# Kernel optimization log

Measured on AMD Instinct MI355X. Metric: run time of the kernel, lower is better.

## Reference

```python
import jax, jax.numpy as jnp
import numpy as np

B, S, I, E, D = 64, 512, 64, 256, 256  # batch, src_len, input_size, enc_hid, dec_hid


def _lstm_cell(h, c, x, Wih, Whh, b):
    # PyTorch LSTM gate order: i, f, g, o ; b = b_ih + b_hh combined
    z = x @ Wih.T + h @ Whh.T + b
    i, f, g, o = jnp.split(z, 4, axis=-1)
    c = jax.nn.sigmoid(f) * c + jax.nn.sigmoid(i) * jnp.tanh(g)
    h = jax.nn.sigmoid(o) * jnp.tanh(c)
    return h, c


def _run_lstm(x, h0, c0, Wih, Whh, b):
    # x: [B,S,I] -> outputs [B,S,H]
    def step(carry, xt):
        h, c = _lstm_cell(carry[0], carry[1], xt, Wih, Whh, b)
        return (h, c), h
    _, ys = jax.lax.scan(step, (h0, c0), jnp.swapaxes(x, 0, 1))
    return jnp.swapaxes(ys, 0, 1)


def _forward(x, enc_h0, enc_c0, dec_h0, dec_c0, Wih_f, Whh_f, b_f, Wih_b, Whh_b, b_b,
             W_attn, b_attn, v, Wih_d, Whh_d, b_d, W_lin, b_lin):
    b_, s_ = x.shape[0], x.shape[1]
    # bidirectional encoder
    out_f = _run_lstm(x, enc_h0[0], enc_c0[0], Wih_f, Whh_f, b_f)
    out_b = _run_lstm(x[:, ::-1, :], enc_h0[1], enc_c0[1], Wih_b, Whh_b, b_b)[:, ::-1, :]
    enc_out = jnp.concatenate([out_f, out_b], axis=-1)  # [B,S,2E]
    h0d, c0d = dec_h0[0], dec_c0[0]  # decoder re-starts from these EVERY step (faithful)

    @jax.checkpoint
    def dec_step(carry, _):
        y, h_attn = carry  # y: [B,1], h_attn: [B,D]
        dh = h_attn.shape[-1]
        cat = jnp.concatenate(
            [jnp.broadcast_to(h_attn[:, None, :], (b_, s_, dh)), enc_out], axis=-1)
        energy = jnp.tanh(cat @ W_attn.T + b_attn)              # [B,S,D]
        attn = jax.nn.softmax(jnp.einsum('d,bsd->bs', v, energy), axis=1)
        context = jnp.einsum('bs,bse->be', attn, enc_out)       # [B,2E]
        dec_in = jnp.concatenate([y, context], axis=-1)         # [B,1+2E]
        h_new, _c = _lstm_cell(h0d, c0d, dec_in, Wih_d, Whh_d, b_d)
        y_new = jnp.concatenate([h_new, context], axis=-1) @ W_lin.T + b_lin  # [B,1]
        return (y_new, h_new), y_new

    y0 = jnp.zeros((b_, 1), dtype=x.dtype)
    _, ys = jax.lax.scan(dec_step, (y0, h0d), None, length=s_)  # [S,B,1]
    # output_size == 1, so torch's cat-then-[:,1:] equals the stacked per-step ys
    return jnp.swapaxes(ys, 0, 1).reshape(b_, s_)


def setup_inputs() -> dict:
    key = jax.random.key(0)
    ks = jax.random.split(key, 20)
    W = 0.05  # weight scale ~ torch default init magnitude
    rn = lambda k, sh, s: jax.random.normal(k, sh, dtype=jnp.float32) * s
    return {
        'x': rn(ks[0], (B, S, I), 1.0),
        'enc_h0': rn(ks[1], (2, B, E), 1.0),
        'enc_c0': rn(ks[2], (2, B, E), 1.0),
        'dec_h0': rn(ks[3], (1, B, D), 1.0),
        'dec_c0': rn(ks[4], (1, B, D), 1.0),
        'Wih_f': rn(ks[5], (4 * E, I), W),
        'Whh_f': rn(ks[6], (4 * E, E), W),
        'b_f': rn(ks[7], (4 * E,), W),
        'Wih_b': rn(ks[8], (4 * E, I), W),
        'Whh_b': rn(ks[9], (4 * E, E), W),
        'b_b': rn(ks[10], (4 * E,), W),
        'W_attn': rn(ks[11], (D, D + 2 * E), W),
        'b_attn': rn(ks[12], (D,), W),
        'v': jax.random.uniform(ks[13], (D,), dtype=jnp.float32),
        'Wih_d': rn(ks[14], (4 * D, 2 * E + 1), W),
        'Whh_d': rn(ks[15], (4 * D, D), W),
        'b_d': rn(ks[16], (4 * D,), W),
        'W_lin': rn(ks[17], (1, 2 * E + D), W),
        'b_lin': rn(ks[18], (1,), W),
    }


def reference(x, enc_h0, enc_c0, dec_h0, dec_c0, Wih_f, Whh_f, b_f, Wih_b, Whh_b, b_b,
              W_attn, b_attn, v, Wih_d, Whh_d, b_d, W_lin, b_lin):
    return _forward(x, enc_h0, enc_c0, dec_h0, dec_c0, Wih_f, Whh_f, b_f,
                    Wih_b, Whh_b, b_b, W_attn, b_attn, v, Wih_d, Whh_d, b_d,
                    W_lin, b_lin)
```

## Files before the change

### kernel.cpp

```cpp
#include <hip/hip_runtime.h>
#include <hip/hip_bf16.h>

#define NB 64
#define NS 512
#define NI 64
#define NE 256
#define ND 256
#define N4E 1024
#define N4D 1024
#define NTE 512
#define G 4
#define SLICE 128
#define CELLS 64

__device__ __forceinline__ float fsig(float x){
    return __fdividef(1.f, 1.f + __expf(-x));
}
__device__ __forceinline__ float ftanh(float x){
    x = fminf(10.f, fmaxf(-10.f, x));
    float e = __expf(2.f*x);
    return 1.f - __fdividef(2.f, e + 1.f);
}
__device__ __forceinline__ float wave_sum(float v){
    #pragma unroll
    for (int o=32;o>0;o>>=1) v += __shfl_xor(v, o, 64);
    return v;
}
__device__ __forceinline__ float wave_max(float v){
    #pragma unroll
    for (int o=32;o>0;o>>=1) v = fmaxf(v, __shfl_xor(v, o, 64));
    return v;
}
__device__ __forceinline__ float blo(unsigned u){ return __uint_as_float(u<<16); }
__device__ __forceinline__ float bhi(unsigned u){ return __uint_as_float(u & 0xffff0000u); }
__device__ __forceinline__ unsigned short bfbits(float f){
    __hip_bfloat16 h = __float2bfloat16(f);
    return *(unsigned short*)&h;
}
__device__ __forceinline__ float ld_agf(const float* p){
    return __hip_atomic_load(p, __ATOMIC_RELAXED, __HIP_MEMORY_SCOPE_AGENT);
}
__device__ __forceinline__ void st_agf(float* p, float v){
    __hip_atomic_store(p, v, __ATOMIC_RELAXED, __HIP_MEMORY_SCOPE_AGENT);
}

__device__ __forceinline__ void groupbar(unsigned* flags, int b, int q,
                                         unsigned tgt, int tid){
    __syncthreads();
    if (tid == 0)
        __hip_atomic_store(&flags[b*4+q], tgt, __ATOMIC_RELAXED, __HIP_MEMORY_SCOPE_AGENT);
    if (tid < 4){
        while (__hip_atomic_load(&flags[b*4+tid], __ATOMIC_RELAXED,
                                 __HIP_MEMORY_SCOPE_AGENT) < tgt)
            __builtin_amdgcn_s_sleep(1);
    }
    __syncthreads();
}

__global__ void k_transpose(float* __restrict__ dst, const float* __restrict__ src,
                            int R, int C, int ld, int off){
    int idx = blockIdx.x*256 + threadIdx.x;
    if (idx >= R*C) return;
    int r = idx / C, c = idx - r*C;
    dst[(size_t)c*R + r] = src[(size_t)r*ld + off + c];
}
__global__ void k_transpose16(__hip_bfloat16* __restrict__ dst, const float* __restrict__ src,
                              int R, int C, int ld, int off){
    int idx = blockIdx.x*256 + threadIdx.x;
    if (idx >= R*C) return;
    int r = idx / C, c = idx - r*C;
    dst[(size_t)c*R + r] = __float2bfloat16(src[(size_t)r*ld + off + c]);
}

__global__ void k_pack_wy(float* __restrict__ wy, const float* __restrict__ Wih_d){
    int j = blockIdx.x*256 + threadIdx.x;
    if (j < N4D) wy[j] = Wih_d[(size_t)j*(NTE+1)];
}

__global__ void k_pack_wdtg(__hip_bfloat16* __restrict__ dst, const float* __restrict__ Wih_d){
    int idx = blockIdx.x*256 + threadIdx.x;
    int q = idx >> 17, rem = idx & 131071;
    int e = rem >> 8, jj = rem & 255;
    int j = ((jj>>6)<<8) + (q<<6) + (jj&63);
    dst[idx] = __float2bfloat16(Wih_d[(size_t)j*(NTE+1) + 1 + e]);
}

__global__ void k_zc(float* __restrict__ zc, const float* __restrict__ WhhTd,
                     const float* __restrict__ h0d, const float* __restrict__ b_d){
    int b = blockIdx.x, tid = threadIdx.x;
    __shared__ float h0[ND];
    if (tid < ND) h0[tid] = h0d[b*ND + tid];
    __syncthreads();
    for (int j = tid; j < N4D; j += 256){
        float acc = b_d[j];
        #pragma unroll 8
        for (int d=0; d<ND; ++d) acc = fmaf(h0[d], WhhTd[d*N4D + j], acc);
        zc[b*N4D + j] = acc;
    }
}

__global__ void k_dec_init(float* __restrict__ hG, float* __restrict__ yG,
                           unsigned* __restrict__ flags, const float* __restrict__ dec_h0){
    int b = blockIdx.x, tid = threadIdx.x;
    hG[b*ND + tid] = dec_h0[b*ND + tid];
    if (tid < G) yG[b*G + tid] = 0.f;
    if (tid < G) flags[b*G + tid] = 0u;
}

__global__ __launch_bounds__(1024) void k_enc(
    const float* __restrict__ x, const float* __restrict__ eh0, const float* __restrict__ ec0,
    const unsigned* __restrict__ whhTf, const unsigned* __restrict__ wihTf, const float* __restrict__ bf,
    const unsigned* __restrict__ whhTb, const unsigned* __restrict__ wihTb, const float* __restrict__ bb,
    unsigned* __restrict__ eo32)
{
    int bid = blockIdx.x;
    int b = bid & 63, dir = bid >> 6;
    int tid = threadIdx.x;
    int j2 = tid & 511, kh = tid >> 9;
    const unsigned* whh = dir ? whhTb : whhTf;
    const unsigned* wih = dir ? wihTb : wihTf;
    const float* bias = dir ? bb : bf;

    __shared__ __align__(16) float h_l[NE];
    __shared__ __align__(16) float xt[2][NI];
    __shared__ float zp0[N4E], zp1[N4E];

    float2 bias2 = make_float2(0.f, 0.f);
    if (kh == 0) bias2 = ((const float2*)bias)[j2];

    float cst = 0.f;
    if (tid < NE){
        h_l[tid] = eh0[(dir*NB+b)*NE + tid];
        cst      = ec0[(dir*NB+b)*NE + tid];
    }
    {
        int st0 = dir ? (NS-1) : 0;
        if (tid < 16) ((float4*)xt[0])[tid] = ((const float4*)(x + ((size_t)b*NS+st0)*NI))[tid];
    }
    __syncthreads();

    const unsigned* wihK = wih + (size_t)(kh*32)*512 + j2;
    const unsigned* whhK = whh + (size_t)(kh*128)*512 + j2;
    float* zpme = kh ? zp1 : zp0;

    for (int t=0;t<NS;++t){
        int st = dir ? (NS-1-t) : t;
        float4 xpre = make_float4(0.f,0.f,0.f,0.f);
        if (t+1 < NS && tid < 16){
            int stn = dir ? (NS-2-t) : (t+1);
            xpre = ((const float4*)(x + ((size_t)b*NS+stn)*NI))[tid];
        }
        const float* xc = xt[t&1];
        float x0=bias2.x, y0=bias2.y, x1=0.f, y1=0.f;
        #pragma unroll 8
        for (int ii=0; ii<32; ii+=2){
            int i = kh*32 + ii;
            unsigned wa = wihK[(size_t)ii*512];
            unsigned wb = wihK[(size_t)(ii+1)*512];
            float xa = xc[i], xb = xc[i+1];
            x0 = fmaf(xa, blo(wa), x0); y0 = fmaf(xa, bhi(wa), y0);
            x1 = fmaf(xb, blo(wb), x1); y1 = fmaf(xb, bhi(wb), y1);
        }
        #pragma unroll 8
        for (int dd=0; dd<128; dd+=2){
            int d = kh*128 + dd;
            unsigned wa = whhK[(size_t)dd*512];
            unsigned wb = whhK[(size_t)(dd+1)*512];
            float ha = h_l[d], hb = h_l[d+1];
            x0 = fmaf(ha, blo(wa), x0); y0 = fmaf(ha, bhi(wa), y0);
            x1 = fmaf(hb, blo(wb), x1); y1 = fmaf(hb, bhi(wb), y1);
        }
        ((float2*)zpme)[j2] = make_float2(x0+x1, y0+y1);
        if (t+1 < NS && tid < 16) ((float4*)xt[(t+1)&1])[tid] = xpre;
        __syncthreads();
        if (tid < NE){
            int c = tid;
            float zi = zp0[c]        + zp1[c];
            float zf = zp0[NE+c]     + zp1[NE+c];
            float zg = zp0[2*NE+c]   + zp1[2*NE+c];
            float zo = zp0[3*NE+c]   + zp1[3*NE+c];
            cst = fsig(zf)*cst + fsig(zi)*ftanh(zg);
            float hn = fsig(zo)*ftanh(cst);
            h_l[c] = hn;
            ((unsigned short*)eo32)[((size_t)b*NS+st)*NTE + dir*NE + c] = bfbits(hn);
        }
        __syncthreads();
    }
}

__global__ __launch_bounds__(256) void k_encproj(const unsigned* __restrict__ eo32,
        const float* __restrict__ WeT, const float* __restrict__ b_attn,
        unsigned short* __restrict__ ep_pk16){
    int b = blockIdx.y, s0 = blockIdx.x*16, tid = threadIdx.x;
    __shared__ float tile[16*NTE];
    {
        const unsigned* eop = eo32 + (size_t)(b*NS + s0)*256;
        for (int k=0;k<32;++k){
            int wi = k*256 + tid;
            unsigned w = eop[wi];
            int sl = wi>>8, ew = wi&255;
            tile[sl*NTE + 2*ew]   = blo(w);
            tile[sl*NTE + 2*ew+1] = bhi(w);
        }
    }
    __syncthreads();
    float acc[16];
    float ba = b_attn[tid];
    #pragma unroll
    for (int sl=0;sl<16;++sl) acc[sl]=ba;
    #pragma unroll 4
    for (int e4=0;e4<128;++e4){
        float w0 = WeT[(4*e4+0)*ND+tid];
        float w1 = WeT[(4*e4+1)*ND+tid];
        float w2 = WeT[(4*e4+2)*ND+tid];
        float w3 = WeT[(4*e4+3)*ND+tid];
        #pragma unroll
        for (int sl=0;sl<16;++sl){
            const float4 tv = *(const float4*)&tile[sl*NTE + 4*e4];
            acc[sl] = fmaf(tv.x,w0,fmaf(tv.y,w1,fmaf(tv.z,w2,fmaf(tv.w,w3,acc[sl]))));
        }
    }
    #pragma unroll
    for (int sl=0;sl<16;++sl){
        int s = s0+sl;
        size_t wdi = ((size_t)(b*4 + (s>>7))*128 + (tid>>1))*128 + (s&127);
        ep_pk16[wdi*2 + (tid&1)] = bfbits(acc[sl]);
    }
}

__global__ __launch_bounds__(1024, 4) void k_dec(
    const unsigned* __restrict__ eo32,
    const unsigned* __restrict__ ep_pk,
    const unsigned* __restrict__ WhTp,
    const float* __restrict__ v,
    const float* __restrict__ zc, const float* __restrict__ wy,
    const unsigned* __restrict__ WdTp_all,
    const float* __restrict__ dec_c0,
    const float* __restrict__ W_lin, const float* __restrict__ b_lin,
    float* __restrict__ hG, float* __restrict__ yG,
    float* __restrict__ ctxG, float* __restrict__ msG,
    unsigned* __restrict__ flags,
    float* __restrict__ out)
{
    int bid = blockIdx.x;
    int b = bid & 63, q = bid >> 6;
    int tid = threadIdx.x;

    __shared__ unsigned ep_lds[16384];
    __shared__ float part[2048];
    __shared__ float h_l[ND];
    __shared__ float2 hv[ND];
    __shared__ float v_l[ND];
    __shared__ float scores_l[SLICE];
    __shared__ float ctx_l[NTE];
    __shared__ float z_l[256], zc_l[256], wy_l[256];
    __shared__ float c0_l[CELLS], wlh_l[CELLS], wlc_l[SLICE];
    __shared__ float msbuf[8];
    __shared__ float wred[16];
    __shared__ float smax, yprev;

    const unsigned* WdTp = WdTp_all + (size_t)q*NTE*128;

    for (int i=tid; i<16384; i+=1024)
        ep_lds[i] = ep_pk[(size_t)(b*4+q)*16384 + i];
    unsigned eo_reg[32];
    {
        int ep2 = tid & 255, sq = tid >> 8;
        const unsigned* eop = eo32 + (size_t)(b*NS + q*SLICE + sq*32)*256 + ep2;
        #pragma unroll
        for (int ss=0; ss<32; ++ss) eo_reg[ss] = eop[(size_t)ss*256];
    }
    if (tid < 256){
        int jj = tid;
        int j = ((jj>>6)<<8) + (q<<6) + (jj&63);
        zc_l[jj] = zc[b*N4D + j];
        wy_l[jj] = wy[j];
        v_l[tid] = v[tid];
    }
    if (tid < CELLS){
        c0_l[tid]  = dec_c0[b*ND + q*CELLS + tid];
        wlh_l[tid] = W_lin[q*CELLS + tid];
    }
    if (tid < SLICE) wlc_l[tid] = W_lin[ND + q*SLICE + tid];
    float blin = b_lin[0];
    __syncthreads();

    for (int t=0; t<NS; ++t){
        if (tid < ND) h_l[tid] = ld_agf(&hG[b*ND + tid]);
        if (tid == 0){
            float y = 0.f;
            if (t > 0){
                y = blin + ld_agf(&yG[b*G+0]) + ld_agf(&yG[b*G+1])
                         + ld_agf(&yG[b*G+2]) + ld_agf(&yG[b*G+3]);
                if (q == 0) out[(size_t)b*NS + (t-1)] = y;
            }
            yprev = y;
        }
        __syncthreads();
        {
            int d2 = tid & 127, kq = tid >> 7;
            float ax = 0.f, ay = 0.f;
            #pragma unroll 8
            for (int kk=0; kk<32; ++kk){
                int k = kq*32 + kk;
                unsigned w = WhTp[k*128 + d2];
                float hvv = h_l[k];
                ax = fmaf(hvv, blo(w), ax); ay = fmaf(hvv, bhi(w), ay);
            }
            ((float2*)part)[kq*128 + d2] = make_float2(ax, ay);
        }
        __syncthreads();
        if (tid < ND){
            float s = 0.f;
            #pragma unroll
            for (int r=0;r<8;++r) s += part[r*256 + tid];
            hv[tid] = make_float2(v_l[tid], s);
        }
        __syncthreads();
        {
            int sl = tid & 127, dg = tid >> 7;
            float sc = 0.f;
            const unsigned* epl = ep_lds + dg*16*128 + sl;
            #pragma unroll
            for (int k16=0; k16<16; ++k16){
                unsigned w = epl[k16*128];
                int d = dg*32 + 2*k16;
                float2 a0 = hv[d], a1 = hv[d+1];
                sc += a0.x*ftanh(blo(w) + a0.y) + a1.x*ftanh(bhi(w) + a1.y);
            }
            part[dg*128 + sl] = sc;
        }
        __syncthreads();
        if (tid < SLICE){
            float s = 0.f;
            #pragma unroll
            for (int r=0;r<8;++r) s += part[r*128 + tid];
            part[1024 + tid] = s;
            float wm = wave_max(s);
            if ((tid&63)==0) wred[tid>>6] = wm;
        }
        __syncthreads();
        if (tid == 0) smax = fmaxf(wred[0], wred[1]);
        __syncthreads();
        if (tid < SLICE){
            float ev = __expf(part[1024 + tid] - smax);
            scores_l[tid] = ev;
            float s = wave_sum(ev);
            if ((tid&63)==0) wred[2+(tid>>6)] = s;
        }
        __syncthreads();
        if (tid == 0){
            st_agf(&msG[(b*G+q)*2+0], smax);
            st_agf(&msG[(b*G+q)*2+1], wred[2]+wred[3]);
        }
        {
            int ep2 = tid & 255, sq = tid >> 8;
            float ax = 0.f, ay = 0.f;
            #pragma unroll
            for (int ss=0; ss<32; ++ss){
                unsigned w = eo_reg[ss];
                float sc = scores_l[sq*32 + ss];
                ax = fmaf(sc, blo(w), ax); ay = fmaf(sc, bhi(w), ay);
            }
            ((float2*)part)[sq*256 + ep2] = make_float2(ax, ay);
        }
        __syncthreads();
        if (tid < NTE){
            float s = part[tid] + part[512+tid] + part[1024+tid] + part[1536+tid];
            st_agf(&ctxG[(size_t)(b*G+q)*NTE + tid], s);
        }
        groupbar(flags, b, q, (unsigned)(2*t+1), tid);
        float cg0=0.f, cg1=0.f, cg2=0.f, cg3=0.f;
        if (tid < 2*G) msbuf[tid] = ld_agf(&msG[b*G*2 + tid]);
        if (tid < NTE){
            const float* cg = ctxG + (size_t)b*G*NTE + tid;
            cg0 = ld_agf(cg);        cg1 = ld_agf(cg+NTE);
            cg2 = ld_agf(cg+2*NTE);  cg3 = ld_agf(cg+3*NTE);
        }
        __syncthreads();
        float mm = fmaxf(fmaxf(msbuf[0], msbuf[2]), fmaxf(msbuf[4], msbuf[6]));
        float w0 = __expf(msbuf[0]-mm), w1 = __expf(msbuf[2]-mm),
              w2 = __expf(msbuf[4]-mm), w3 = __expf(msbuf[6]-mm);
        float inv = __fdividef(1.f, msbuf[1]*w0 + msbuf[3]*w1 + msbuf[5]*w2 + msbuf[7]*w3);
        if (tid < NTE)
            ctx_l[tid] = (cg0*w0 + cg1*w1 + cg2*w2 + cg3*w3) * inv;
        __syncthreads();
        {
            int jj2 = tid & 127, eq = tid >> 7;
            float ax = 0.f, ay = 0.f;
            #pragma unroll 8
            for (int ee=0; ee<64; ++ee){
                int e = eq*64 + ee;
                unsigned w = WdTp[e*128 + jj2];
                float cv = ctx_l[e];
                ax = fmaf(cv, blo(w), ax); ay = fmaf(cv, bhi(w), ay);
            }
            ((float2*)part)[eq*128 + jj2] = make_float2(ax, ay);
        }
        __syncthreads();
        if (tid < 256){
            float s = zc_l[tid] + yprev*wy_l[tid];
            #pragma unroll
            for (int r=0;r<8;++r) s += part[r*256 + tid];
            z_l[tid] = s;
        }
        __syncthreads();
        float yp = 0.f;
        if (tid < CELLS){
            float zi=z_l[tid], zf=z_l[64+tid], zg=z_l[128+tid], zo=z_l[192+tid];
            float cn = fsig(zf)*c0_l[tid] + fsig(zi)*ftanh(zg);
            float hn = fsig(zo)*ftanh(cn);
            st_agf(&hG[b*ND + q*CELLS + tid], hn);
            yp = hn * wlh_l[tid];
        } else if (tid < CELLS + SLICE){
            yp = ctx_l[q*SLICE + (tid - CELLS)] * wlc_l[tid - CELLS];
        }
        {
            float s = wave_sum(yp);
            if ((tid&63)==0 && tid < 192) wred[8+(tid>>6)] = s;
        }
        __syncthreads();
        if (tid == 0) st_agf(&yG[b*G + q], wred[8]+wred[9]+wred[10]);
        groupbar(flags, b, q, (unsigned)(2*t+2), tid);
    }
    if (q == 0 && tid == 0){
        out[(size_t)b*NS + (NS-1)] = blin + ld_agf(&yG[b*G+0]) + ld_agf(&yG[b*G+1])
                                          + ld_agf(&yG[b*G+2]) + ld_agf(&yG[b*G+3]);
    }
}

extern "C" void kernel_launch(void* const* d_in, const int* in_sizes, int n_in,
                              void* d_out, int out_size, void* d_ws, size_t ws_size,
                              hipStream_t stream){
    const float* x      = (const float*)d_in[0];
    const float* enc_h0 = (const float*)d_in[1];
    const float* enc_c0 = (const float*)d_in[2];
    const float* dec_h0 = (const float*)d_in[3];
    const float* dec_c0 = (const float*)d_in[4];
    const float* Wih_f  = (const float*)d_in[5];
    const float* Whh_f  = (const float*)d_in[6];
    const float* b_f    = (const float*)d_in[7];
    const float* Wih_b  = (const float*)d_in[8];
    const float* Whh_b  = (const float*)d_in[9];
    const float* b_b    = (const float*)d_in[10];
    const float* W_attn = (const float*)d_in[11];
    const float* b_attn = (const float*)d_in[12];
    const float* v      = (const float*)d_in[13];
    const float* Wih_d  = (const float*)d_in[14];
    const float* Whh_d  = (const float*)d_in[15];
    const float* b_d    = (const float*)d_in[16];
    const float* W_lin  = (const float*)d_in[17];
    const float* b_lin  = (const float*)d_in[18];
    float* out = (float*)d_out;
    char* ws   = (char*)d_ws;

    size_t off = 0;
    auto alloc = [&](size_t bytes)->size_t{ size_t o = off; off += (bytes + 255) & ~(size_t)255; return o; };
    size_t o_eo16   = alloc((size_t)NB*NS*NTE*2);
    size_t o_eppk   = alloc((size_t)NB*G*128*128*4);
    size_t o_WihTf  = alloc((size_t)NI*N4E*2);
    size_t o_WhhTf  = alloc((size_t)NE*N4E*2);
    size_t o_WihTb  = alloc((size_t)NI*N4E*2);
    size_t o_WhhTb  = alloc((size_t)NE*N4E*2);
    size_t o_WhT16  = alloc((size_t)ND*ND*2);
    size_t o_WeT    = alloc((size_t)NTE*ND*4);
    size_t o_WdTg   = alloc((size_t)G*NTE*256*2);
    size_t o_WhhTd  = alloc((size_t)ND*N4D*4);
    size_t o_zc     = alloc((size_t)NB*N4D*4);
    size_t o_wy     = alloc((size_t)N4D*4);
    size_t o_hG     = alloc((size_t)NB*ND*4);
    size_t o_yG     = alloc((size_t)NB*G*4);
    size_t o_ctxG   = alloc((size_t)NB*G*NTE*4);
    size_t o_msG    = alloc((size_t)NB*G*2*4);
    size_t o_flags  = alloc((size_t)NB*G*4);
    if (ws_size < off) return;

    auto F   = [&](size_t o)->float*{ return (float*)(ws + o); };
    auto U32 = [&](size_t o)->unsigned*{ return (unsigned*)(ws + o); };
    auto H16 = [&](size_t o)->__hip_bfloat16*{ return (__hip_bfloat16*)(ws + o); };

    auto T32 = [&](size_t dsto, const float* src, int R, int C, int ld, int offc){
        int n = R*C;
        k_transpose<<<dim3((n+255)/256), dim3(256), 0, stream>>>(F(dsto), src, R, C, ld, offc);
    };
    auto T16 = [&](size_t dsto, const float* src, int R, int C, int ld, int offc){
        int n = R*C;
        k_transpose16<<<dim3((n+255)/256), dim3(256), 0, stream>>>(H16(dsto), src, R, C, ld, offc);
    };
    T16(o_WihTf, Wih_f, N4E, NI, NI, 0);
    T16(o_WhhTf, Whh_f, N4E, NE, NE, 0);
    T16(o_WihTb, Wih_b, N4E, NI, NI, 0);
    T16(o_WhhTb, Whh_b, N4E, NE, NE, 0);
    T16(o_WhT16, W_attn, ND, ND, ND+NTE, 0);
    T32(o_WeT,   W_attn, ND, NTE, ND+NTE, ND);
    T32(o_WhhTd, Whh_d, N4D, ND, ND, 0);
    k_pack_wdtg<<<dim3((G*NTE*256)/256), dim3(256), 0, stream>>>(H16(o_WdTg), Wih_d);
    k_pack_wy<<<dim3(4), dim3(256), 0, stream>>>(F(o_wy), Wih_d);
    k_zc<<<dim3(NB), dim3(256), 0, stream>>>(F(o_zc), F(o_WhhTd), dec_h0, b_d);
    k_dec_init<<<dim3(NB), dim3(256), 0, stream>>>(F(o_hG), F(o_yG), (unsigned*)(ws+o_flags), dec_h0);

    k_enc<<<dim3(2*NB), dim3(1024), 0, stream>>>(x, enc_h0, enc_c0,
        U32(o_WhhTf), U32(o_WihTf), b_f, U32(o_WhhTb), U32(o_WihTb), b_b, U32(o_eo16));

    k_encproj<<<dim3(NS/16, NB), dim3(256), 0, stream>>>(U32(o_eo16), F(o_WeT), b_attn,
        (unsigned short*)(ws+o_eppk));

    k_dec<<<dim3(NB*G), dim3(1024), 0, stream>>>(U32(o_eo16), U32(o_eppk),
        U32(o_WhT16), v, F(o_zc), F(o_wy), U32(o_WdTg), dec_c0, W_lin, b_lin,
        F(o_hG), F(o_yG), F(o_ctxG), F(o_msG), (unsigned*)(ws+o_flags), out);
}
```

Baseline: 18.35 ms.

## Run decoder with one block per batch, dropping cross-block barriers

The decoder's per-batch work is no longer split across four cooperating blocks that synchronise through global flags and atomics twice per step. One 1024-thread block now handles a whole batch row with uint4-vectorised bf16 weight loads, and softmax and context are reduced locally. This removes the inter-block barrier latency and global traffic on every step. In exchange only 64 blocks run, encoder outputs stream from global or L2 instead of living in registers or LDS, and per-block work grows fourfold. The tanh clamp is also dropped.

```diff
diff --git a/kernel.cpp b/kernel.cpp
--- a/kernel.cpp
+++ b/kernel.cpp
@@ -9,17 +9,12 @@
 #define N4E 1024
 #define N4D 1024
 #define NTE 512
-#define G 4
-#define SLICE 128
-#define CELLS 64
 
 __device__ __forceinline__ float fsig(float x){
     return __fdividef(1.f, 1.f + __expf(-x));
 }
 __device__ __forceinline__ float ftanh(float x){
-    x = fminf(10.f, fmaxf(-10.f, x));
-    float e = __expf(2.f*x);
-    return 1.f - __fdividef(2.f, e + 1.f);
+    return 1.f - __fdividef(2.f, 1.f + __expf(2.f*x));
 }
 __device__ __forceinline__ float wave_sum(float v){
     #pragma unroll
@@ -36,25 +31,6 @@
 __device__ __forceinline__ unsigned short bfbits(float f){
     __hip_bfloat16 h = __float2bfloat16(f);
     return *(unsigned short*)&h;
-}
-__device__ __forceinline__ float ld_agf(const float* p){
-    return __hip_atomic_load(p, __ATOMIC_RELAXED, __HIP_MEMORY_SCOPE_AGENT);
-}
-__device__ __forceinline__ void st_agf(float* p, float v){
-    __hip_atomic_store(p, v, __ATOMIC_RELAXED, __HIP_MEMORY_SCOPE_AGENT);
-}
-
-__device__ __forceinline__ void groupbar(unsigned* flags, int b, int q,
-                                         unsigned tgt, int tid){
-    __syncthreads();
-    if (tid == 0)
-        __hip_atomic_store(&flags[b*4+q], tgt, __ATOMIC_RELAXED, __HIP_MEMORY_SCOPE_AGENT);
-    if (tid < 4){
-        while (__hip_atomic_load(&flags[b*4+tid], __ATOMIC_RELAXED,
-                                 __HIP_MEMORY_SCOPE_AGENT) < tgt)
-            __builtin_amdgcn_s_sleep(1);
-    }
-    __syncthreads();
 }
 
 __global__ void k_transpose(float* __restrict__ dst, const float* __restrict__ src,
@@ -75,14 +51,6 @@
 __global__ void k_pack_wy(float* __restrict__ wy, const float* __restrict__ Wih_d){
     int j = blockIdx.x*256 + threadIdx.x;
     if (j < N4D) wy[j] = Wih_d[(size_t)j*(NTE+1)];
-}
-
-__global__ void k_pack_wdtg(__hip_bfloat16* __restrict__ dst, const float* __restrict__ Wih_d){
-    int idx = blockIdx.x*256 + threadIdx.x;
-    int q = idx >> 17, rem = idx & 131071;
-    int e = rem >> 8, jj = rem & 255;
-    int j = ((jj>>6)<<8) + (q<<6) + (jj&63);
-    dst[idx] = __float2bfloat16(Wih_d[(size_t)j*(NTE+1) + 1 + e]);
 }
 
 __global__ void k_zc(float* __restrict__ zc, const float* __restrict__ WhhTd,
@@ -97,14 +65,6 @@
         for (int d=0; d<ND; ++d) acc = fmaf(h0[d], WhhTd[d*N4D + j], acc);
         zc[b*N4D + j] = acc;
     }
-}
-
-__global__ void k_dec_init(float* __restrict__ hG, float* __restrict__ yG,
-                           unsigned* __restrict__ flags, const float* __restrict__ dec_h0){
-    int b = blockIdx.x, tid = threadIdx.x;
-    hG[b*ND + tid] = dec_h0[b*ND + tid];
-    if (tid < G) yG[b*G + tid] = 0.f;
-    if (tid < G) flags[b*G + tid] = 0u;
 }
 
 __global__ __launch_bounds__(1024) void k_enc(
@@ -223,209 +183,198 @@
     #pragma unroll
     for (int sl=0;sl<16;++sl){
         int s = s0+sl;
-        size_t wdi = ((size_t)(b*4 + (s>>7))*128 + (tid>>1))*128 + (s&127);
+        size_t wdi = ((size_t)(b*128) + (tid>>1))*NS + s;
         ep_pk16[wdi*2 + (tid&1)] = bfbits(acc[sl]);
     }
 }
 
-__global__ __launch_bounds__(1024, 4) void k_dec(
-    const unsigned* __restrict__ eo32,
-    const unsigned* __restrict__ ep_pk,
-    const unsigned* __restrict__ WhTp,
+__global__ __launch_bounds__(1024, 1) void k_dec(
+    const uint4* __restrict__ eo4,
+    const uint4* __restrict__ ep4,
+    const uint4* __restrict__ whT4,
+    const uint4* __restrict__ wdT4,
     const float* __restrict__ v,
     const float* __restrict__ zc, const float* __restrict__ wy,
-    const unsigned* __restrict__ WdTp_all,
-    const float* __restrict__ dec_c0,
+    const float* __restrict__ dec_h0, const float* __restrict__ dec_c0,
     const float* __restrict__ W_lin, const float* __restrict__ b_lin,
-    float* __restrict__ hG, float* __restrict__ yG,
-    float* __restrict__ ctxG, float* __restrict__ msG,
-    unsigned* __restrict__ flags,
     float* __restrict__ out)
 {
-    int bid = blockIdx.x;
-    int b = bid & 63, q = bid >> 6;
-    int tid = threadIdx.x;
-
-    __shared__ unsigned ep_lds[16384];
-    __shared__ float part[2048];
+    int b = blockIdx.x, tid = threadIdx.x;
+
+    __shared__ float part[8192];
+    __shared__ float2 hv[ND];
     __shared__ float h_l[ND];
-    __shared__ float2 hv[ND];
-    __shared__ float v_l[ND];
-    __shared__ float scores_l[SLICE];
+    __shared__ float scores_l[NS];
     __shared__ float ctx_l[NTE];
-    __shared__ float z_l[256], zc_l[256], wy_l[256];
-    __shared__ float c0_l[CELLS], wlh_l[CELLS], wlc_l[SLICE];
-    __shared__ float msbuf[8];
+    __shared__ float z_l[N4D], zc_l[N4D], wy_l[N4D];
+    __shared__ float c0_l[ND], wlh_l[ND], wlc_l[NTE];
     __shared__ float wred[16];
-    __shared__ float smax, yprev;
-
-    const unsigned* WdTp = WdTp_all + (size_t)q*NTE*128;
-
-    for (int i=tid; i<16384; i+=1024)
-        ep_lds[i] = ep_pk[(size_t)(b*4+q)*16384 + i];
-    unsigned eo_reg[32];
-    {
-        int ep2 = tid & 255, sq = tid >> 8;
-        const unsigned* eop = eo32 + (size_t)(b*NS + q*SLICE + sq*32)*256 + ep2;
-        #pragma unroll
-        for (int ss=0; ss<32; ++ss) eo_reg[ss] = eop[(size_t)ss*256];
-    }
-    if (tid < 256){
-        int jj = tid;
-        int j = ((jj>>6)<<8) + (q<<6) + (jj&63);
-        zc_l[jj] = zc[b*N4D + j];
-        wy_l[jj] = wy[j];
-        v_l[tid] = v[tid];
-    }
-    if (tid < CELLS){
-        c0_l[tid]  = dec_c0[b*ND + q*CELLS + tid];
-        wlh_l[tid] = W_lin[q*CELLS + tid];
-    }
-    if (tid < SLICE) wlc_l[tid] = W_lin[ND + q*SLICE + tid];
+    __shared__ float yprevS;
+
+    zc_l[tid] = zc[b*N4D + tid];
+    wy_l[tid] = wy[tid];
+    if (tid < ND){
+        hv[tid]    = make_float2(v[tid], 0.f);
+        h_l[tid]   = dec_h0[b*ND + tid];
+        c0_l[tid]  = dec_c0[b*ND + tid];
+        wlh_l[tid] = W_lin[tid];
+    }
+    if (tid < NTE) wlc_l[tid] = W_lin[ND + tid];
+    if (tid == 0) yprevS = 0.f;
     float blin = b_lin[0];
     __syncthreads();
 
+    const uint4* epb = ep4 + (size_t)b*128*128;
+    const uint4* eob = eo4 + (size_t)b*NS*64;
+
     for (int t=0; t<NS; ++t){
-        if (tid < ND) h_l[tid] = ld_agf(&hG[b*ND + tid]);
-        if (tid == 0){
-            float y = 0.f;
-            if (t > 0){
-                y = blin + ld_agf(&yG[b*G+0]) + ld_agf(&yG[b*G+1])
-                         + ld_agf(&yG[b*G+2]) + ld_agf(&yG[b*G+3]);
-                if (q == 0) out[(size_t)b*NS + (t-1)] = y;
-            }
-            yprev = y;
-        }
-        __syncthreads();
-        {
-            int d2 = tid & 127, kq = tid >> 7;
-            float ax = 0.f, ay = 0.f;
-            #pragma unroll 8
-            for (int kk=0; kk<32; ++kk){
-                int k = kq*32 + kk;
-                unsigned w = WhTp[k*128 + d2];
+        {
+            int d4 = tid & 31, kq = tid >> 5;
+            float ax[8];
+            #pragma unroll
+            for (int j=0;j<8;++j) ax[j]=0.f;
+            #pragma unroll
+            for (int kk=0; kk<8; ++kk){
+                int k = kq*8 + kk;
+                uint4 w = whT4[k*32 + d4];
                 float hvv = h_l[k];
-                ax = fmaf(hvv, blo(w), ax); ay = fmaf(hvv, bhi(w), ay);
-            }
-            ((float2*)part)[kq*128 + d2] = make_float2(ax, ay);
+                ax[0]=fmaf(hvv,blo(w.x),ax[0]); ax[1]=fmaf(hvv,bhi(w.x),ax[1]);
+                ax[2]=fmaf(hvv,blo(w.y),ax[2]); ax[3]=fmaf(hvv,bhi(w.y),ax[3]);
+                ax[4]=fmaf(hvv,blo(w.z),ax[4]); ax[5]=fmaf(hvv,bhi(w.z),ax[5]);
+                ax[6]=fmaf(hvv,blo(w.w),ax[6]); ax[7]=fmaf(hvv,bhi(w.w),ax[7]);
+            }
+            #pragma unroll
+            for (int j=0;j<8;++j) part[kq*256 + d4*8 + j] = ax[j];
         }
         __syncthreads();
         if (tid < ND){
             float s = 0.f;
             #pragma unroll
-            for (int r=0;r<8;++r) s += part[r*256 + tid];
-            hv[tid] = make_float2(v_l[tid], s);
-        }
-        __syncthreads();
-        {
-            int sl = tid & 127, dg = tid >> 7;
-            float sc = 0.f;
-            const unsigned* epl = ep_lds + dg*16*128 + sl;
-            #pragma unroll
-            for (int k16=0; k16<16; ++k16){
-                unsigned w = epl[k16*128];
-                int d = dg*32 + 2*k16;
-                float2 a0 = hv[d], a1 = hv[d+1];
-                sc += a0.x*ftanh(blo(w) + a0.y) + a1.x*ftanh(bhi(w) + a1.y);
-            }
-            part[dg*128 + sl] = sc;
-        }
-        __syncthreads();
-        if (tid < SLICE){
+            for (int g=0; g<32; ++g) s += part[g*256 + tid];
+            hv[tid].y = s;
+        }
+        __syncthreads();
+        {
+            int s4 = tid & 127, dh = tid >> 7;
+            float sc[4];
+            #pragma unroll
+            for (int j=0;j<4;++j) sc[j]=0.f;
+            #pragma unroll
+            for (int k=0; k<16; ++k){
+                int dp = dh*16 + k;
+                uint4 w = epb[dp*128 + s4];
+                float2 a0 = hv[2*dp], a1 = hv[2*dp+1];
+                const unsigned* ws = &w.x;
+                #pragma unroll
+                for (int su=0; su<4; ++su){
+                    unsigned ww = ws[su];
+                    sc[su] += a0.x*ftanh(blo(ww)+a0.y) + a1.x*ftanh(bhi(ww)+a1.y);
+                }
+            }
+            #pragma unroll
+            for (int su=0; su<4; ++su) part[dh*512 + s4*4 + su] = sc[su];
+        }
+        __syncthreads();
+        {
+            float scval = -1e30f;
+            if (tid < NS){
+                scval = 0.f;
+                #pragma unroll
+                for (int g=0; g<8; ++g) scval += part[g*512 + tid];
+            }
+            float wm = wave_max(scval);
+            if ((tid&63)==0 && tid < NS) wred[tid>>6] = wm;
+            __syncthreads();
+            if (tid < NS){
+                float mm = wred[0];
+                #pragma unroll
+                for (int g=1; g<8; ++g) mm = fmaxf(mm, wred[g]);
+                float ev = __expf(scval - mm);
+                scores_l[tid] = ev;
+                float sw = wave_sum(ev);
+                if ((tid&63)==0) wred[8+(tid>>6)] = sw;
+            }
+        }
+        __syncthreads();
+        {
+            int e4 = tid & 63, sq = tid >> 6;
+            float ax[8];
+            #pragma unroll
+            for (int j=0;j<8;++j) ax[j]=0.f;
+            #pragma unroll 8
+            for (int ss=0; ss<32; ++ss){
+                int s = sq*32 + ss;
+                uint4 w = eob[s*64 + e4];
+                float p = scores_l[s];
+                ax[0]=fmaf(p,blo(w.x),ax[0]); ax[1]=fmaf(p,bhi(w.x),ax[1]);
+                ax[2]=fmaf(p,blo(w.y),ax[2]); ax[3]=fmaf(p,bhi(w.y),ax[3]);
+                ax[4]=fmaf(p,blo(w.z),ax[4]); ax[5]=fmaf(p,bhi(w.z),ax[5]);
+                ax[6]=fmaf(p,blo(w.w),ax[6]); ax[7]=fmaf(p,bhi(w.w),ax[7]);
+            }
+            #pragma unroll
+            for (int j=0;j<8;++j) part[sq*512 + e4*8 + j] = ax[j];
+        }
+        __syncthreads();
+        if (tid < NTE){
+            float den = wred[8];
+            #pragma unroll
+            for (int g=9; g<16; ++g) den += wred[g];
+            float inv = __fdividef(1.f, den);
             float s = 0.f;
             #pragma unroll
-            for (int r=0;r<8;++r) s += part[r*128 + tid];
-            part[1024 + tid] = s;
-            float wm = wave_max(s);
-            if ((tid&63)==0) wred[tid>>6] = wm;
-        }
-        __syncthreads();
-        if (tid == 0) smax = fmaxf(wred[0], wred[1]);
-        __syncthreads();
-        if (tid < SLICE){
-            float ev = __expf(part[1024 + tid] - smax);
-            scores_l[tid] = ev;
-            float s = wave_sum(ev);
-            if ((tid&63)==0) wred[2+(tid>>6)] = s;
-        }
-        __syncthreads();
-        if (tid == 0){
-            st_agf(&msG[(b*G+q)*2+0], smax);
-            st_agf(&msG[(b*G+q)*2+1], wred[2]+wred[3]);
-        }
-        {
-            int ep2 = tid & 255, sq = tid >> 8;
-            float ax = 0.f, ay = 0.f;
-            #pragma unroll
-            for (int ss=0; ss<32; ++ss){
-                unsigned w = eo_reg[ss];
-                float sc = scores_l[sq*32 + ss];
-                ax = fmaf(sc, blo(w), ax); ay = fmaf(sc, bhi(w), ay);
-            }
-            ((float2*)part)[sq*256 + ep2] = make_float2(ax, ay);
-        }
-        __syncthreads();
-        if (tid < NTE){
-            float s = part[tid] + part[512+tid] + part[1024+tid] + part[1536+tid];
-            st_agf(&ctxG[(size_t)(b*G+q)*NTE + tid], s);
-        }
-        groupbar(flags, b, q, (unsigned)(2*t+1), tid);
-        float cg0=0.f, cg1=0.f, cg2=0.f, cg3=0.f;
-        if (tid < 2*G) msbuf[tid] = ld_agf(&msG[b*G*2 + tid]);
-        if (tid < NTE){
-            const float* cg = ctxG + (size_t)b*G*NTE + tid;
-            cg0 = ld_agf(cg);        cg1 = ld_agf(cg+NTE);
-            cg2 = ld_agf(cg+2*NTE);  cg3 = ld_agf(cg+3*NTE);
-        }
-        __syncthreads();
-        float mm = fmaxf(fmaxf(msbuf[0], msbuf[2]), fmaxf(msbuf[4], msbuf[6]));
-        float w0 = __expf(msbuf[0]-mm), w1 = __expf(msbuf[2]-mm),
-              w2 = __expf(msbuf[4]-mm), w3 = __expf(msbuf[6]-mm);
-        float inv = __fdividef(1.f, msbuf[1]*w0 + msbuf[3]*w1 + msbuf[5]*w2 + msbuf[7]*w3);
-        if (tid < NTE)
-            ctx_l[tid] = (cg0*w0 + cg1*w1 + cg2*w2 + cg3*w3) * inv;
-        __syncthreads();
-        {
-            int jj2 = tid & 127, eq = tid >> 7;
-            float ax = 0.f, ay = 0.f;
-            #pragma unroll 8
+            for (int g=0; g<16; ++g) s += part[g*512 + tid];
+            ctx_l[tid] = s * inv;
+        }
+        __syncthreads();
+        {
+            int j4 = tid & 127, eq = tid >> 7;
+            float ax[8];
+            #pragma unroll
+            for (int j=0;j<8;++j) ax[j]=0.f;
+            #pragma unroll 16
             for (int ee=0; ee<64; ++ee){
                 int e = eq*64 + ee;
-                unsigned w = WdTp[e*128 + jj2];
+                uint4 w = wdT4[e*128 + j4];
                 float cv = ctx_l[e];
-                ax = fmaf(cv, blo(w), ax); ay = fmaf(cv, bhi(w), ay);
-            }
-            ((float2*)part)[eq*128 + jj2] = make_float2(ax, ay);
-        }
-        __syncthreads();
-        if (tid < 256){
-            float s = zc_l[tid] + yprev*wy_l[tid];
-            #pragma unroll
-            for (int r=0;r<8;++r) s += part[r*256 + tid];
+                ax[0]=fmaf(cv,blo(w.x),ax[0]); ax[1]=fmaf(cv,bhi(w.x),ax[1]);
+                ax[2]=fmaf(cv,blo(w.y),ax[2]); ax[3]=fmaf(cv,bhi(w.y),ax[3]);
+                ax[4]=fmaf(cv,blo(w.z),ax[4]); ax[5]=fmaf(cv,bhi(w.z),ax[5]);
+                ax[6]=fmaf(cv,blo(w.w),ax[6]); ax[7]=fmaf(cv,bhi(w.w),ax[7]);
+            }
+            #pragma unroll
+            for (int j=0;j<8;++j) part[eq*1024 + j4*8 + j] = ax[j];
+        }
+        __syncthreads();
+        {
+            float s = zc_l[tid] + yprevS*wy_l[tid];
+            #pragma unroll
+            for (int g=0; g<8; ++g) s += part[g*1024 + tid];
             z_l[tid] = s;
         }
         __syncthreads();
         float yp = 0.f;
-        if (tid < CELLS){
-            float zi=z_l[tid], zf=z_l[64+tid], zg=z_l[128+tid], zo=z_l[192+tid];
+        if (tid < ND){
+            float zi=z_l[tid], zf=z_l[ND+tid], zg=z_l[2*ND+tid], zo=z_l[3*ND+tid];
             float cn = fsig(zf)*c0_l[tid] + fsig(zi)*ftanh(zg);
             float hn = fsig(zo)*ftanh(cn);
-            st_agf(&hG[b*ND + q*CELLS + tid], hn);
+            h_l[tid] = hn;
             yp = hn * wlh_l[tid];
-        } else if (tid < CELLS + SLICE){
-            yp = ctx_l[q*SLICE + (tid - CELLS)] * wlc_l[tid - CELLS];
+        } else if (tid < ND + NTE){
+            yp = ctx_l[tid - ND] * wlc_l[tid - ND];
         }
         {
             float s = wave_sum(yp);
-            if ((tid&63)==0 && tid < 192) wred[8+(tid>>6)] = s;
-        }
-        __syncthreads();
-        if (tid == 0) st_agf(&yG[b*G + q], wred[8]+wred[9]+wred[10]);
-        groupbar(flags, b, q, (unsigned)(2*t+2), tid);
-    }
-    if (q == 0 && tid == 0){
-        out[(size_t)b*NS + (NS-1)] = blin + ld_agf(&yG[b*G+0]) + ld_agf(&yG[b*G+1])
-                                          + ld_agf(&yG[b*G+2]) + ld_agf(&yG[b*G+3]);
+            if ((tid&63)==0 && tid < 768) wred[tid>>6] = s;
+        }
+        __syncthreads();
+        if (tid == 0){
+            float y = blin;
+            #pragma unroll
+            for (int g=0; g<12; ++g) y += wred[g];
+            out[(size_t)b*NS + t] = y;
+            yprevS = y;
+        }
+        __syncthreads();
     }
 }
 
@@ -457,26 +406,22 @@
     size_t off = 0;
     auto alloc = [&](size_t bytes)->size_t{ size_t o = off; off += (bytes + 255) & ~(size_t)255; return o; };
     size_t o_eo16   = alloc((size_t)NB*NS*NTE*2);
-    size_t o_eppk   = alloc((size_t)NB*G*128*128*4);
+    size_t o_eppk   = alloc((size_t)NB*128*NS*4);
     size_t o_WihTf  = alloc((size_t)NI*N4E*2);
     size_t o_WhhTf  = alloc((size_t)NE*N4E*2);
     size_t o_WihTb  = alloc((size_t)NI*N4E*2);
     size_t o_WhhTb  = alloc((size_t)NE*N4E*2);
     size_t o_WhT16  = alloc((size_t)ND*ND*2);
     size_t o_WeT    = alloc((size_t)NTE*ND*4);
-    size_t o_WdTg   = alloc((size_t)G*NTE*256*2);
+    size_t o_WdT16  = alloc((size_t)NTE*N4D*2);
     size_t o_WhhTd  = alloc((size_t)ND*N4D*4);
     size_t o_zc     = alloc((size_t)NB*N4D*4);
     size_t o_wy     = alloc((size_t)N4D*4);
-    size_t o_hG     = alloc((size_t)NB*ND*4);
-    size_t o_yG     = alloc((size_t)NB*G*4);
-    size_t o_ctxG   = alloc((size_t)NB*G*NTE*4);
-    size_t o_msG    = alloc((size_t)NB*G*2*4);
-    size_t o_flags  = alloc((size_t)NB*G*4);
     if (ws_size < off) return;
 
     auto F   = [&](size_t o)->float*{ return (float*)(ws + o); };
     auto U32 = [&](size_t o)->unsigned*{ return (unsigned*)(ws + o); };
+    auto U4  = [&](size_t o)->uint4*{ return (uint4*)(ws + o); };
     auto H16 = [&](size_t o)->__hip_bfloat16*{ return (__hip_bfloat16*)(ws + o); };
 
     auto T32 = [&](size_t dsto, const float* src, int R, int C, int ld, int offc){
@@ -493,11 +438,10 @@
     T16(o_WhhTb, Whh_b, N4E, NE, NE, 0);
     T16(o_WhT16, W_attn, ND, ND, ND+NTE, 0);
     T32(o_WeT,   W_attn, ND, NTE, ND+NTE, ND);
+    T16(o_WdT16, Wih_d, N4D, NTE, NTE+1, 1);
     T32(o_WhhTd, Whh_d, N4D, ND, ND, 0);
-    k_pack_wdtg<<<dim3((G*NTE*256)/256), dim3(256), 0, stream>>>(H16(o_WdTg), Wih_d);
     k_pack_wy<<<dim3(4), dim3(256), 0, stream>>>(F(o_wy), Wih_d);
     k_zc<<<dim3(NB), dim3(256), 0, stream>>>(F(o_zc), F(o_WhhTd), dec_h0, b_d);
-    k_dec_init<<<dim3(NB), dim3(256), 0, stream>>>(F(o_hG), F(o_yG), (unsigned*)(ws+o_flags), dec_h0);
 
     k_enc<<<dim3(2*NB), dim3(1024), 0, stream>>>(x, enc_h0, enc_c0,
         U32(o_WhhTf), U32(o_WihTf), b_f, U32(o_WhhTb), U32(o_WihTb), b_b, U32(o_eo16));
@@ -505,7 +449,6 @@
     k_encproj<<<dim3(NS/16, NB), dim3(256), 0, stream>>>(U32(o_eo16), F(o_WeT), b_attn,
         (unsigned short*)(ws+o_eppk));
 
-    k_dec<<<dim3(NB*G), dim3(1024), 0, stream>>>(U32(o_eo16), U32(o_eppk),
-        U32(o_WhT16), v, F(o_zc), F(o_wy), U32(o_WdTg), dec_c0, W_lin, b_lin,
-        F(o_hG), F(o_yG), F(o_ctxG), F(o_msG), (unsigned*)(ws+o_flags), out);
-}
+    k_dec<<<dim3(NB), dim3(1024), 0, stream>>>(U4(o_eo16), U4(o_eppk),
+        U4(o_WhT16), U4(o_WdT16), v, F(o_zc), F(o_wy), dec_h0, dec_c0, W_lin, b_lin, out);
+}
```

After: 57.24 ms. +212.0%, slower.
